# Performance work log

Measured on AMD Instinct MI355X. Metric: run time of the kernel, lower is better.

Reference implementation:

```python
import jax, jax.numpy as jnp
import numpy as np

B, T, E, G, A, D, H1, H2 = 64, 500, 256, 256, 128, 400, 256, 128
MAX_STEPS, R = 500, 5


def setup_inputs() -> dict:
    key = jax.random.key(0)
    ks = jax.random.split(key, 12)
    s = lambda k, shape: jax.random.normal(k, shape, jnp.float32) * 0.05
    return dict(
        enc_feat=jax.random.normal(ks[0], (B, T, E), jnp.float32),
        W_p1=s(ks[1], (D, H1)), b_p1=jnp.zeros((H1,), jnp.float32),
        W_p2=s(ks[2], (H1, H2)), b_p2=jnp.zeros((H2,), jnp.float32),
        # GRU cell (input = prenet_out + context = H2+E)
        W_ix=s(ks[3], (H2 + E, 3 * G)), W_ih=s(ks[4], (G, 3 * G)),
        b_ix=jnp.zeros((3 * G,), jnp.float32), b_ih=jnp.zeros((3 * G,), jnp.float32),
        # Bahdanau MLP attention: v^T tanh(W_dec h + W_enc e + b)
        W_dec=s(ks[5], (G, A)), W_enc=s(ks[6], (E, A)),
        b_attn=jnp.zeros((A,), jnp.float32), v_attn=s(ks[7], (A,)),
        # output projection [G+E] -> D, softmaxed per R chunks
        W_out=s(ks[8], (G + E, D)), b_out=jnp.zeros((D,), jnp.float32),
    )


def reference(enc_feat, W_p1, b_p1, W_p2, b_p2, W_ix, W_ih, b_ix, b_ih,
              W_dec, W_enc, b_attn, v_attn, W_out, b_out):
    # precompute encoder-side attention projection once [B,T,A]
    enc_proj = enc_feat @ W_enc

    def gru_cell(x, h):
        gi = x @ W_ix + b_ix  # [B,3G]
        gh = h @ W_ih + b_ih
        i_r, i_z, i_n = jnp.split(gi, 3, axis=-1)
        h_r, h_z, h_n = jnp.split(gh, 3, axis=-1)
        r = jax.nn.sigmoid(i_r + h_r)
        z = jax.nn.sigmoid(i_z + h_z)
        n = jnp.tanh(i_n + r * h_n)
        return (1.0 - z) * n + z * h

    def step(carry, _):
        pred, h, context = carry
        # prenet (eval: no dropout)
        x = jax.nn.relu(jax.nn.relu(pred @ W_p1 + b_p1) @ W_p2 + b_p2)  # [B,H2]
        h = gru_cell(jnp.concatenate([x, context], axis=-1), h)  # [B,G]
        score = jnp.einsum('bta,a->bt',
                           jnp.tanh(enc_proj + (h @ W_dec + b_attn)[:, None, :]),
                           v_attn)  # [B,T]
        attn = jax.nn.softmax(score, axis=-1)
        context = jnp.einsum('bt,bte->be', attn, enc_feat)  # [B,E]
        raw = jnp.concatenate([h, context], axis=-1) @ W_out + b_out  # [B,D]
        pred = jax.nn.softmax(raw.reshape(B, R, D // R), axis=-1).reshape(B, D)
        return (pred, h, context), (pred, attn)

    init = (jnp.zeros((B, D), enc_feat.dtype),
            jnp.zeros((B, G), enc_feat.dtype),
            jnp.zeros((B, E), enc_feat.dtype))
    _, (pred_seq, attn_record) = jax.lax.scan(step, init, None, length=MAX_STEPS)
    # scan stacks on leading axis: [S,B,.] -> [B,S,.]
    return jnp.transpose(pred_seq, (1, 0, 2)), jnp.transpose(attn_record, (1, 0, 2))
```

## Files before the change

kernel.cpp:

```cpp
#include <hip/hip_runtime.h>
#include <math.h>

constexpr int Bb = 64, Tt = 500, Ee = 256, Aa = 128, Dd = 400;
constexpr int STEPS = 500, Rr = 5;

constexpr size_t WS_ENCPROJ_F = 0;
constexpr size_t WS_STAGE_F   = (size_t)Bb * Tt * Aa;
constexpr size_t WS_CNT_F     = WS_STAGE_F + (size_t)Bb * 2048;
constexpr int SG_L1 = 0, SG_H = 256, SG_SC = 512, SG_CTX = 1024, SG_RAW = 1280;
constexpr int SG_STRIDE = 2048;

__global__ __launch_bounds__(512)
void k_encproj(const float* __restrict__ enc_feat,
               const float* __restrict__ W_enc,
               float* __restrict__ enc_proj) {
  __shared__ float sFeat[16][256];
  const int b = blockIdx.x, tg = blockIdx.y;
  const int t0 = tg * 16;
  const int tid = threadIdx.x;

  #pragma unroll
  for (int i = 0; i < 8; ++i) {
    int idx = tid + i * 512;
    int r = idx >> 8, c = idx & 255;
    int t = t0 + r;
    sFeat[r][c] = (t < Tt) ? enc_feat[((size_t)b * Tt + t) * Ee + c] : 0.0f;
  }
  __syncthreads();

  const int a = tid & 127, tl = tid >> 7;
  float acc0 = 0.f, acc1 = 0.f, acc2 = 0.f, acc3 = 0.f;
  #pragma unroll 4
  for (int k = 0; k < Ee; ++k) {
    float w = W_enc[k * Aa + a];
    acc0 = fmaf(sFeat[tl][k],      w, acc0);
    acc1 = fmaf(sFeat[tl + 4][k],  w, acc1);
    acc2 = fmaf(sFeat[tl + 8][k],  w, acc2);
    acc3 = fmaf(sFeat[tl + 12][k], w, acc3);
  }
  float accs[4] = {acc0, acc1, acc2, acc3};
  #pragma unroll
  for (int i = 0; i < 4; ++i) {
    int t = t0 + tl + 4 * i;
    if (t < Tt) enc_proj[((size_t)b * Tt + t) * Aa + a] = accs[i];
  }
}

__device__ __forceinline__ float sigmoid_acc(float x) {
  float e = __expf(-x);
  return 1.0f / (1.0f + e);
}
__device__ __forceinline__ float tanh_acc(float x) {
  float cx = fminf(9.5f, fmaxf(-9.5f, x));
  float e = __expf(2.0f * cx);
  return (e - 1.0f) / (e + 1.0f);
}
__device__ __forceinline__ float tanh_fast(float x) {
  float cx = fminf(9.5f, fmaxf(-9.5f, x));
  float e = __expf(2.0f * cx);
  return (e - 1.0f) * __builtin_amdgcn_rcpf(e + 1.0f);
}

__device__ __forceinline__ void rowsync(unsigned* __restrict__ cnt, int tid, int& target) {
  __syncthreads();
  target += 4;
  if (tid == 0) {
    __hip_atomic_fetch_add(cnt, 1u, __ATOMIC_RELEASE, __HIP_MEMORY_SCOPE_AGENT);
    while (__hip_atomic_load(cnt, __ATOMIC_RELAXED, __HIP_MEMORY_SCOPE_AGENT) < (unsigned)target) { }
    __threadfence();
  }
  __syncthreads();
}

__global__ __launch_bounds__(512)
void k_decoder(const float* __restrict__ enc_feat,
               const float* __restrict__ enc_proj,
               float* __restrict__ stage, unsigned* __restrict__ cntbase,
               const float* __restrict__ W_p1, const float* __restrict__ b_p1,
               const float* __restrict__ W_p2, const float* __restrict__ b_p2,
               const float* __restrict__ W_ix, const float* __restrict__ W_ih,
               const float* __restrict__ b_ix, const float* __restrict__ b_ih,
               const float* __restrict__ W_dec, const float* __restrict__ b_attn,
               const float* __restrict__ v_attn,
               const float* __restrict__ W_out, const float* __restrict__ b_out,
               float* __restrict__ pred_out, float* __restrict__ attn_out) {
  __shared__ __align__(16) float sPred[400];
  __shared__ __align__(16) float sIn[384];
  __shared__ __align__(16) float sL1[256];
  __shared__ __align__(16) float sCat[512];
  __shared__ __align__(16) float sSd[128];
  __shared__ __align__(16) float sScore[512];
  __shared__ __align__(16) float sRaw[400];
  __shared__ __align__(16) float sTmp[2048];
  __shared__ float sRed[8];

  float* sH = sCat;

  const int bid = blockIdx.x;
  const int r = bid & 63, j = bid >> 6;
  const int tid = threadIdx.x;
  const int lane = tid & 63, wid = tid >> 6;
  const int l4 = tid & 3;

  float* stg = stage + (size_t)r * SG_STRIDE;
  unsigned* cnt = cntbase + r * 64;
  int target = 0;

  for (int i = tid; i < 400; i += 512) sPred[i] = 0.f;
  if (tid < 256) { sH[tid] = 0.f; sIn[128 + tid] = 0.f; }

  float4 vq[8];
  #pragma unroll
  for (int i = 0; i < 8; ++i) vq[i] = *(const float4*)(v_attn + 4 * (l4 + 4 * i));

  float bP1 = 0.f, bR = 0.f, bZ = 0.f, bIN = 0.f, bHN = 0.f;
  if (tid < 64) {
    int c = 64 * j + tid;
    bP1 = b_p1[c];
    bR  = b_ix[c]       + b_ih[c];
    bZ  = b_ix[256 + c] + b_ih[256 + c];
    bIN = b_ix[512 + c];
    bHN = b_ih[512 + c];
  }
  float bP2 = 0.f, bAt = 0.f;
  if (tid < 128) { bP2 = b_p2[tid]; bAt = b_attn[tid]; }
  float bOut = 0.f;
  if (tid < 100) bOut = b_out[100 * j + tid];

  const int p1q = tid & 15, p1s = tid >> 4;
  const int p1k0 = 12 * p1s + min(p1s, 16);
  const int p1k1 = p1k0 + ((p1s < 16) ? 13 : 12);
  const float* p1W = W_p1 + (64 * j + 4 * p1q) + (size_t)p1k0 * 256;
  const int p2q = tid & 31, p2s = tid >> 5;
  const float* p2W = W_p2 + 4 * p2q + (size_t)(16 * p2s) * 128;
  const float* p6W = W_dec + 4 * p2q + (size_t)(16 * p2s) * 128;
  const float* gW = W_ix;
  const float* gx = sIn;
  if (tid < 288) {
    int q = tid % 48, s = tid / 48;
    int g = q >> 4, lq = q & 15;
    gW = W_ix + (size_t)(s * 64) * 768 + (g * 256 + 64 * j + 4 * lq);
    gx = sIn + s * 64;
  } else if (tid < 480) {
    int t2 = tid - 288, q = t2 % 48, s = t2 / 48;
    int g = q >> 4, lq = q & 15;
    gW = W_ih + (size_t)(s * 64) * 768 + (g * 256 + 64 * j + 4 * lq);
    gx = sH + s * 64;
  }
  const bool gAct = tid < 480;
  const int p10q = tid % 25, p10s = tid / 25;
  const int p10k0 = 25 * p10s + min(p10s, 12);
  const int p10k1 = p10k0 + ((p10s < 12) ? 26 : 25);
  const float* p10W = W_out + (100 * j + 4 * p10q) + (size_t)p10k0 * 400;
  const int e9q = tid & 15, t9s = tid >> 4;
  const int t9a = t9s * 16;
  const int t9b = (t9a + 16 < Tt) ? t9a + 16 : Tt;
  const float* fb9 = enc_feat + (size_t)r * Tt * Ee + (64 * j + 4 * e9q);
  const int tt7 = tid >> 2;
  const float* ep7 = enc_proj + ((size_t)r * Tt + (125 * j + tt7)) * Aa;

  __syncthreads();

  for (int t = 0; t < STEPS; ++t) {
    {
      float4 acc = {0.f, 0.f, 0.f, 0.f};
      const float* W = p1W;
      #pragma unroll 8
      for (int k = p1k0; k < p1k1; ++k, W += 256) {
        float xv = sPred[k];
        float4 w = *(const float4*)W;
        acc.x = fmaf(xv, w.x, acc.x); acc.y = fmaf(xv, w.y, acc.y);
        acc.z = fmaf(xv, w.z, acc.z); acc.w = fmaf(xv, w.w, acc.w);
      }
      *(float4*)&sTmp[tid * 4] = acc;
    }
    __syncthreads();
    if (tid < 64) {
      float v = bP1;
      #pragma unroll
      for (int s = 0; s < 32; ++s) v += sTmp[(16 * s + (tid >> 2)) * 4 + (tid & 3)];
      stg[SG_L1 + 64 * j + tid] = fmaxf(v, 0.f);
    }
    rowsync(cnt, tid, target);
    if (tid < 256) sL1[tid] = stg[SG_L1 + tid];
    __syncthreads();

    {
      float4 acc = {0.f, 0.f, 0.f, 0.f};
      const float* W = p2W;
      const float* xp = sL1 + 16 * p2s;
      #pragma unroll 8
      for (int k = 0; k < 16; ++k, W += 128) {
        float xv = xp[k];
        float4 w = *(const float4*)W;
        acc.x = fmaf(xv, w.x, acc.x); acc.y = fmaf(xv, w.y, acc.y);
        acc.z = fmaf(xv, w.z, acc.z); acc.w = fmaf(xv, w.w, acc.w);
      }
      *(float4*)&sTmp[tid * 4] = acc;
    }
    __syncthreads();
    if (tid < 128) {
      float v = bP2;
      #pragma unroll
      for (int s = 0; s < 16; ++s) v += sTmp[(32 * s + (tid >> 2)) * 4 + (tid & 3)];
      sIn[tid] = fmaxf(v, 0.f);
    }
    __syncthreads();

    if (gAct) {
      float4 acc = {0.f, 0.f, 0.f, 0.f};
      const float* W = gW;
      const float* xp = gx;
      #pragma unroll 8
      for (int k = 0; k < 64; ++k, W += 768) {
        float xv = xp[k];
        float4 w = *(const float4*)W;
        acc.x = fmaf(xv, w.x, acc.x); acc.y = fmaf(xv, w.y, acc.y);
        acc.z = fmaf(xv, w.z, acc.z); acc.w = fmaf(xv, w.w, acc.w);
      }
      *(float4*)&sTmp[tid * 4] = acc;
    }
    __syncthreads();
    if (tid < 64) {
      const int cq = tid >> 2, ce = tid & 3;
      float cr = bR, cz = bZ, vin = bIN, vhn = bHN;
      #pragma unroll
      for (int s = 0; s < 6; ++s) {
        cr  += sTmp[(48 * s +      cq) * 4 + ce];
        cz  += sTmp[(48 * s + 16 + cq) * 4 + ce];
        vin += sTmp[(48 * s + 32 + cq) * 4 + ce];
      }
      #pragma unroll
      for (int s = 0; s < 4; ++s) {
        cr  += sTmp[(288 + 48 * s +      cq) * 4 + ce];
        cz  += sTmp[(288 + 48 * s + 16 + cq) * 4 + ce];
        vhn += sTmp[(288 + 48 * s + 32 + cq) * 4 + ce];
      }
      float rg = sigmoid_acc(cr);
      float zg = sigmoid_acc(cz);
      float n  = tanh_acc(vin + rg * vhn);
      stg[SG_H + 64 * j + tid] = (1.f - zg) * n + zg * sH[64 * j + tid];
    }
    rowsync(cnt, tid, target);
    if (tid < 256) sH[tid] = stg[SG_H + tid];
    __syncthreads();

    {
      float4 acc = {0.f, 0.f, 0.f, 0.f};
      const float* W = p6W;
      const float* xp = sH + 16 * p2s;
      #pragma unroll 8
      for (int k = 0; k < 16; ++k, W += 128) {
        float xv = xp[k];
        float4 w = *(const float4*)W;
        acc.x = fmaf(xv, w.x, acc.x); acc.y = fmaf(xv, w.y, acc.y);
        acc.z = fmaf(xv, w.z, acc.z); acc.w = fmaf(xv, w.w, acc.w);
      }
      *(float4*)&sTmp[tid * 4] = acc;
    }
    __syncthreads();
    if (tid < 128) {
      float v = bAt;
      #pragma unroll
      for (int s = 0; s < 16; ++s) v += sTmp[(32 * s + (tid >> 2)) * 4 + (tid & 3)];
      sSd[tid] = v;
    }
    __syncthreads();

    {
      float4 sdq[8];
      #pragma unroll
      for (int i = 0; i < 8; ++i) sdq[i] = *(const float4*)(sSd + 4 * (l4 + 4 * i));
      float acc = 0.f;
      if (tt7 < 125) {
        #pragma unroll
        for (int i = 0; i < 8; ++i) {
          float4 e4 = ((const float4*)ep7)[l4 + 4 * i];
          acc = fmaf(vq[i].x, tanh_fast(e4.x + sdq[i].x), acc);
          acc = fmaf(vq[i].y, tanh_fast(e4.y + sdq[i].y), acc);
          acc = fmaf(vq[i].z, tanh_fast(e4.z + sdq[i].z), acc);
          acc = fmaf(vq[i].w, tanh_fast(e4.w + sdq[i].w), acc);
        }
      }
      acc += __shfl_xor(acc, 1);
      acc += __shfl_xor(acc, 2);
      if (l4 == 0 && tt7 < 125) stg[SG_SC + 125 * j + tt7] = acc;
    }
    rowsync(cnt, tid, target);
    if (tid < Tt) sScore[tid] = stg[SG_SC + tid];
    __syncthreads();

    {
      float val = (tid < Tt) ? sScore[tid] : -3.0e38f;
      float m = val;
      #pragma unroll
      for (int off = 32; off >= 1; off >>= 1) m = fmaxf(m, __shfl_xor(m, off));
      if (lane == 0) sRed[wid] = m;
      __syncthreads();
      float bm = sRed[0];
      #pragma unroll
      for (int w = 1; w < 8; ++w) bm = fmaxf(bm, sRed[w]);
      float e = (tid < Tt) ? __expf(val - bm) : 0.f;
      float ssum = e;
      #pragma unroll
      for (int off = 32; off >= 1; off >>= 1) ssum += __shfl_xor(ssum, off);
      __syncthreads();
      if (lane == 0) sRed[wid] = ssum;
      __syncthreads();
      float S = 0.f;
      #pragma unroll
      for (int w = 0; w < 8; ++w) S += sRed[w];
      if (tid < Tt) {
        float attn = e / S;
        sScore[tid] = attn;
        if (tid >= 125 * j && tid < 125 * (j + 1))
          attn_out[((size_t)r * STEPS + t) * Tt + tid] = attn;
      }
      __syncthreads();
    }

    {
      float4 acc = {0.f, 0.f, 0.f, 0.f};
      #pragma unroll 8
      for (int tt = t9a; tt < t9b; ++tt) {
        float a = sScore[tt];
        float4 f = *(const float4*)(fb9 + (size_t)tt * Ee);
        acc.x = fmaf(a, f.x, acc.x); acc.y = fmaf(a, f.y, acc.y);
        acc.z = fmaf(a, f.z, acc.z); acc.w = fmaf(a, f.w, acc.w);
      }
      *(float4*)&sTmp[tid * 4] = acc;
      __syncthreads();
      if (tid < 64) {
        float v = 0.f;
        #pragma unroll
        for (int s = 0; s < 32; ++s) v += sTmp[(16 * s + (tid >> 2)) * 4 + (tid & 3)];
        stg[SG_CTX + 64 * j + tid] = v;
      }
      rowsync(cnt, tid, target);
      if (tid < 256) {
        float v = stg[SG_CTX + tid];
        sIn[128 + tid] = v;
        sCat[256 + tid] = v;
      }
      __syncthreads();
    }

    if (tid < 500) {
      float4 acc = {0.f, 0.f, 0.f, 0.f};
      const float* W = p10W;
      #pragma unroll 8
      for (int k = p10k0; k < p10k1; ++k, W += 400) {
        float xv = sCat[k];
        float4 w = *(const float4*)W;
        acc.x = fmaf(xv, w.x, acc.x); acc.y = fmaf(xv, w.y, acc.y);
        acc.z = fmaf(xv, w.z, acc.z); acc.w = fmaf(xv, w.w, acc.w);
      }
      *(float4*)&sTmp[tid * 4] = acc;
    }
    __syncthreads();
    if (tid < 100) {
      float v = bOut;
      #pragma unroll
      for (int s = 0; s < 20; ++s) v += sTmp[(25 * s + (tid >> 2)) * 4 + (tid & 3)];
      stg[SG_RAW + 100 * j + tid] = v;
    }
    rowsync(cnt, tid, target);
    if (tid < 400) sRaw[tid] = stg[SG_RAW + tid];
    __syncthreads();

    {
      if (wid < Rr) {
        int d0 = wid * 80 + lane;
        float v0 = sRaw[d0];
        float v1 = (lane < 16) ? sRaw[d0 + 64] : -3.0e38f;
        float m = fmaxf(v0, v1);
        #pragma unroll
        for (int off = 32; off >= 1; off >>= 1) m = fmaxf(m, __shfl_xor(m, off));
        float e0 = __expf(v0 - m);
        float e1 = (lane < 16) ? __expf(v1 - m) : 0.f;
        float s = e0 + e1;
        #pragma unroll
        for (int off = 32; off >= 1; off >>= 1) s += __shfl_xor(s, off);
        float inv = 1.0f / s;
        float p0 = e0 * inv;
        sPred[d0] = p0;
        if (j == 0) pred_out[((size_t)r * STEPS + t) * Dd + d0] = p0;
        if (lane < 16) {
          float p1 = e1 * inv;
          sPred[d0 + 64] = p1;
          if (j == 0) pred_out[((size_t)r * STEPS + t) * Dd + d0 + 64] = p1;
        }
      }
      __syncthreads();
    }
  }
}

extern "C" void kernel_launch(void* const* d_in, const int* in_sizes, int n_in,
                              void* d_out, int out_size, void* d_ws, size_t ws_size,
                              hipStream_t stream) {
  const float* enc_feat = (const float*)d_in[0];
  const float* W_p1  = (const float*)d_in[1];
  const float* b_p1  = (const float*)d_in[2];
  const float* W_p2  = (const float*)d_in[3];
  const float* b_p2  = (const float*)d_in[4];
  const float* W_ix  = (const float*)d_in[5];
  const float* W_ih  = (const float*)d_in[6];
  const float* b_ix  = (const float*)d_in[7];
  const float* b_ih  = (const float*)d_in[8];
  const float* W_dec = (const float*)d_in[9];
  const float* W_enc = (const float*)d_in[10];
  const float* b_attn= (const float*)d_in[11];
  const float* v_attn= (const float*)d_in[12];
  const float* W_out = (const float*)d_in[13];
  const float* b_out = (const float*)d_in[14];

  float* pred_out = (float*)d_out;
  float* attn_out = pred_out + (size_t)Bb * STEPS * Dd;

  float* enc_proj = (float*)d_ws + WS_ENCPROJ_F;
  float* stage    = (float*)d_ws + WS_STAGE_F;
  unsigned* cnt   = (unsigned*)((float*)d_ws + WS_CNT_F);

  hipMemsetAsync(cnt, 0, 64 * 64 * sizeof(unsigned), stream);
  k_encproj<<<dim3(Bb, 32), 512, 0, stream>>>(enc_feat, W_enc, enc_proj);

  void* args[] = {
    (void*)&enc_feat, (void*)&enc_proj, (void*)&stage, (void*)&cnt,
    (void*)&W_p1, (void*)&b_p1, (void*)&W_p2, (void*)&b_p2,
    (void*)&W_ix, (void*)&W_ih, (void*)&b_ix, (void*)&b_ih,
    (void*)&W_dec, (void*)&b_attn, (void*)&v_attn,
    (void*)&W_out, (void*)&b_out, (void*)&pred_out, (void*)&attn_out
  };
  hipLaunchCooperativeKernel(reinterpret_cast<const void*>(k_decoder),
                             dim3(4 * Bb), dim3(512), args, 0, stream);
}
```

Before: 41.89 ms.

## Replicate small matvecs per block and cut cross-block syncs per decoder step

Each of the four blocks per batch row now computes the full prenet layer 1 and output projection redundantly, so the staging exchanges and row barriers for those stages go away. Attention softmax becomes local per block, with only max and sum statistics exchanged, and each block computes a partial context over its own 125 time steps that is then summed across blocks. A double-buffered register prefetch helper replaces the simple weight-streaming dot loops. This trades extra redundant weight traffic and FLOPs per block for fewer grid-level synchronisations per step.

```diff
diff --git a/kernel.cpp b/kernel.cpp
--- a/kernel.cpp
+++ b/kernel.cpp
@@ -7,7 +7,7 @@
 constexpr size_t WS_ENCPROJ_F = 0;
 constexpr size_t WS_STAGE_F   = (size_t)Bb * Tt * Aa;
 constexpr size_t WS_CNT_F     = WS_STAGE_F + (size_t)Bb * 2048;
-constexpr int SG_L1 = 0, SG_H = 256, SG_SC = 512, SG_CTX = 1024, SG_RAW = 1280;
+constexpr int SG_H = 0, SG_STAT = 256, SG_CTXP = 512;
 constexpr int SG_STRIDE = 2048;
 
 __global__ __launch_bounds__(512)
@@ -44,6 +44,55 @@
     int t = t0 + tl + 4 * i;
     if (t < Tt) enc_proj[((size_t)b * Tt + t) * Aa + a] = accs[i];
   }
+}
+
+template<int KS, int NB>
+__device__ __forceinline__ float4 dotq_db(const float* __restrict__ W, const int ldW,
+                                          const float* __restrict__ x) {
+  float4 acc = {0.f, 0.f, 0.f, 0.f};
+  constexpr int NC = KS / NB;
+  constexpr int TL = KS - NC * NB;
+  float4 Abuf[NB], Bbuf[NB > 0 ? NB : 1];
+  if constexpr (NC > 0) {
+    #pragma unroll
+    for (int j = 0; j < NB; ++j) Abuf[j] = *(const float4*)(W + (size_t)j * ldW);
+  }
+  #pragma unroll
+  for (int c = 0; c < NC; ++c) {
+    float4* cur = (c & 1) ? Bbuf : Abuf;
+    float4* nxt = (c & 1) ? Abuf : Bbuf;
+    if (c + 1 < NC) {
+      const float* Wn = W + (size_t)((c + 1) * NB) * ldW;
+      #pragma unroll
+      for (int j = 0; j < NB; ++j) nxt[j] = *(const float4*)(Wn + (size_t)j * ldW);
+    } else if constexpr (TL > 0) {
+      const float* Wn = W + (size_t)(NC * NB) * ldW;
+      #pragma unroll
+      for (int j = 0; j < TL; ++j) nxt[j] = *(const float4*)(Wn + (size_t)j * ldW);
+    }
+    const float* xb = x + c * NB;
+    #pragma unroll
+    for (int j = 0; j < NB; ++j) {
+      float xv = xb[j];
+      acc.x = fmaf(xv, cur[j].x, acc.x); acc.y = fmaf(xv, cur[j].y, acc.y);
+      acc.z = fmaf(xv, cur[j].z, acc.z); acc.w = fmaf(xv, cur[j].w, acc.w);
+    }
+  }
+  if constexpr (TL > 0) {
+    float4* cur = (NC & 1) ? Bbuf : Abuf;
+    if constexpr (NC == 0) {
+      #pragma unroll
+      for (int j = 0; j < TL; ++j) cur[j] = *(const float4*)(W + (size_t)j * ldW);
+    }
+    const float* xb = x + NC * NB;
+    #pragma unroll
+    for (int j = 0; j < TL; ++j) {
+      float xv = xb[j];
+      acc.x = fmaf(xv, cur[j].x, acc.x); acc.y = fmaf(xv, cur[j].y, acc.y);
+      acc.z = fmaf(xv, cur[j].z, acc.z); acc.w = fmaf(xv, cur[j].w, acc.w);
+    }
+  }
+  return acc;
 }
 
 __device__ __forceinline__ float sigmoid_acc(float x) {
@@ -89,7 +138,7 @@
   __shared__ __align__(16) float sL1[256];
   __shared__ __align__(16) float sCat[512];
   __shared__ __align__(16) float sSd[128];
-  __shared__ __align__(16) float sScore[512];
+  __shared__ __align__(16) float sScore[128];
   __shared__ __align__(16) float sRaw[400];
   __shared__ __align__(16) float sTmp[2048];
   __shared__ float sRed[8];
@@ -113,10 +162,11 @@
   #pragma unroll
   for (int i = 0; i < 8; ++i) vq[i] = *(const float4*)(v_attn + 4 * (l4 + 4 * i));
 
-  float bP1 = 0.f, bR = 0.f, bZ = 0.f, bIN = 0.f, bHN = 0.f;
+  float bP1 = 0.f;
+  if (tid < 256) bP1 = b_p1[tid];
+  float bR = 0.f, bZ = 0.f, bIN = 0.f, bHN = 0.f;
   if (tid < 64) {
     int c = 64 * j + tid;
-    bP1 = b_p1[c];
     bR  = b_ix[c]       + b_ih[c];
     bZ  = b_ix[256 + c] + b_ih[256 + c];
     bIN = b_ix[512 + c];
@@ -125,79 +175,46 @@
   float bP2 = 0.f, bAt = 0.f;
   if (tid < 128) { bP2 = b_p2[tid]; bAt = b_attn[tid]; }
   float bOut = 0.f;
-  if (tid < 100) bOut = b_out[100 * j + tid];
-
-  const int p1q = tid & 15, p1s = tid >> 4;
-  const int p1k0 = 12 * p1s + min(p1s, 16);
-  const int p1k1 = p1k0 + ((p1s < 16) ? 13 : 12);
-  const float* p1W = W_p1 + (64 * j + 4 * p1q) + (size_t)p1k0 * 256;
-  const int p2q = tid & 31, p2s = tid >> 5;
-  const float* p2W = W_p2 + 4 * p2q + (size_t)(16 * p2s) * 128;
-  const float* p6W = W_dec + 4 * p2q + (size_t)(16 * p2s) * 128;
+  if (tid < 400) bOut = b_out[tid];
+
+  const float* p1W = W_p1 + 4 * (tid & 63) + (size_t)((tid >> 6) * 50) * 256;
+  const float* p1x = sPred + (tid >> 6) * 50;
+  const float* p2W = W_p2 + 4 * (tid & 31) + (size_t)((tid >> 5) * 16) * 128;
+  const float* p2x = sL1 + (tid >> 5) * 16;
+  const float* p6W = W_dec + 4 * (tid & 31) + (size_t)((tid >> 5) * 16) * 128;
+  const float* p6x = sH + (tid >> 5) * 16;
   const float* gW = W_ix;
   const float* gx = sIn;
-  if (tid < 288) {
+  const bool gAct = tid < 480;
+  if (gAct) {
     int q = tid % 48, s = tid / 48;
-    int g = q >> 4, lq = q & 15;
-    gW = W_ix + (size_t)(s * 64) * 768 + (g * 256 + 64 * j + 4 * lq);
-    gx = sIn + s * 64;
-  } else if (tid < 480) {
-    int t2 = tid - 288, q = t2 % 48, s = t2 / 48;
-    int g = q >> 4, lq = q & 15;
-    gW = W_ih + (size_t)(s * 64) * 768 + (g * 256 + 64 * j + 4 * lq);
-    gx = sH + s * 64;
-  }
-  const bool gAct = tid < 480;
-  const int p10q = tid % 25, p10s = tid / 25;
-  const int p10k0 = 25 * p10s + min(p10s, 12);
-  const int p10k1 = p10k0 + ((p10s < 12) ? 26 : 25);
-  const float* p10W = W_out + (100 * j + 4 * p10q) + (size_t)p10k0 * 400;
-  const int e9q = tid & 15, t9s = tid >> 4;
-  const int t9a = t9s * 16;
-  const int t9b = (t9a + 16 < Tt) ? t9a + 16 : Tt;
-  const float* fb9 = enc_feat + (size_t)r * Tt * Ee + (64 * j + 4 * e9q);
+    int col = 256 * (q >> 4) + 64 * j + 4 * (q & 15);
+    if (s < 6) { gW = W_ix + (size_t)(64 * s) * 768 + col; gx = sIn + 64 * s; }
+    else       { gW = W_ih + (size_t)(64 * (s - 6)) * 768 + col; gx = sH + 64 * (s - 6); }
+  }
+  const int q10 = tid % 100, s10 = tid / 100;
+  const float* p10W = W_out + 4 * q10 + (size_t)(128 * s10) * 400;
+  const float* p10x = sCat + 128 * s10;
   const int tt7 = tid >> 2;
   const float* ep7 = enc_proj + ((size_t)r * Tt + (125 * j + tt7)) * Aa;
+  const int e9q = tid & 63, t9s = tid >> 6;
+  const int t9a = t9s * 16;
+  const float* fb9 = enc_feat + ((size_t)r * Tt + 125 * j + t9a) * Ee + 4 * e9q;
 
   __syncthreads();
 
   for (int t = 0; t < STEPS; ++t) {
-    {
-      float4 acc = {0.f, 0.f, 0.f, 0.f};
-      const float* W = p1W;
-      #pragma unroll 8
-      for (int k = p1k0; k < p1k1; ++k, W += 256) {
-        float xv = sPred[k];
-        float4 w = *(const float4*)W;
-        acc.x = fmaf(xv, w.x, acc.x); acc.y = fmaf(xv, w.y, acc.y);
-        acc.z = fmaf(xv, w.z, acc.z); acc.w = fmaf(xv, w.w, acc.w);
-      }
-      *(float4*)&sTmp[tid * 4] = acc;
-    }
-    __syncthreads();
-    if (tid < 64) {
+    { float4 a = dotq_db<50, 8>(p1W, 256, p1x); *(float4*)&sTmp[tid * 4] = a; }
+    __syncthreads();
+    if (tid < 256) {
       float v = bP1;
       #pragma unroll
-      for (int s = 0; s < 32; ++s) v += sTmp[(16 * s + (tid >> 2)) * 4 + (tid & 3)];
-      stg[SG_L1 + 64 * j + tid] = fmaxf(v, 0.f);
-    }
-    rowsync(cnt, tid, target);
-    if (tid < 256) sL1[tid] = stg[SG_L1 + tid];
-    __syncthreads();
-
-    {
-      float4 acc = {0.f, 0.f, 0.f, 0.f};
-      const float* W = p2W;
-      const float* xp = sL1 + 16 * p2s;
-      #pragma unroll 8
-      for (int k = 0; k < 16; ++k, W += 128) {
-        float xv = xp[k];
-        float4 w = *(const float4*)W;
-        acc.x = fmaf(xv, w.x, acc.x); acc.y = fmaf(xv, w.y, acc.y);
-        acc.z = fmaf(xv, w.z, acc.z); acc.w = fmaf(xv, w.w, acc.w);
-      }
-      *(float4*)&sTmp[tid * 4] = acc;
-    }
+      for (int s = 0; s < 8; ++s) v += sTmp[(64 * s + (tid >> 2)) * 4 + (tid & 3)];
+      sL1[tid] = fmaxf(v, 0.f);
+    }
+    __syncthreads();
+
+    { float4 a = dotq_db<16, 16>(p2W, 128, p2x); *(float4*)&sTmp[tid * 4] = a; }
     __syncthreads();
     if (tid < 128) {
       float v = bP2;
@@ -207,35 +224,20 @@
     }
     __syncthreads();
 
-    if (gAct) {
-      float4 acc = {0.f, 0.f, 0.f, 0.f};
-      const float* W = gW;
-      const float* xp = gx;
-      #pragma unroll 8
-      for (int k = 0; k < 64; ++k, W += 768) {
-        float xv = xp[k];
-        float4 w = *(const float4*)W;
-        acc.x = fmaf(xv, w.x, acc.x); acc.y = fmaf(xv, w.y, acc.y);
-        acc.z = fmaf(xv, w.z, acc.z); acc.w = fmaf(xv, w.w, acc.w);
-      }
-      *(float4*)&sTmp[tid * 4] = acc;
-    }
+    if (gAct) { float4 a = dotq_db<64, 8>(gW, 768, gx); *(float4*)&sTmp[tid * 4] = a; }
     __syncthreads();
     if (tid < 64) {
       const int cq = tid >> 2, ce = tid & 3;
       float cr = bR, cz = bZ, vin = bIN, vhn = bHN;
       #pragma unroll
-      for (int s = 0; s < 6; ++s) {
-        cr  += sTmp[(48 * s +      cq) * 4 + ce];
-        cz  += sTmp[(48 * s + 16 + cq) * 4 + ce];
-        vin += sTmp[(48 * s + 32 + cq) * 4 + ce];
-      }
-      #pragma unroll
-      for (int s = 0; s < 4; ++s) {
-        cr  += sTmp[(288 + 48 * s +      cq) * 4 + ce];
-        cz  += sTmp[(288 + 48 * s + 16 + cq) * 4 + ce];
-        vhn += sTmp[(288 + 48 * s + 32 + cq) * 4 + ce];
-      }
+      for (int s = 0; s < 10; ++s) {
+        cr += sTmp[(48 * s +      cq) * 4 + ce];
+        cz += sTmp[(48 * s + 16 + cq) * 4 + ce];
+      }
+      #pragma unroll
+      for (int s = 0; s < 6; ++s) vin += sTmp[(48 * s + 32 + cq) * 4 + ce];
+      #pragma unroll
+      for (int s = 6; s < 10; ++s) vhn += sTmp[(48 * s + 32 + cq) * 4 + ce];
       float rg = sigmoid_acc(cr);
       float zg = sigmoid_acc(cz);
       float n  = tanh_acc(vin + rg * vhn);
@@ -245,19 +247,7 @@
     if (tid < 256) sH[tid] = stg[SG_H + tid];
     __syncthreads();
 
-    {
-      float4 acc = {0.f, 0.f, 0.f, 0.f};
-      const float* W = p6W;
-      const float* xp = sH + 16 * p2s;
-      #pragma unroll 8
-      for (int k = 0; k < 16; ++k, W += 128) {
-        float xv = xp[k];
-        float4 w = *(const float4*)W;
-        acc.x = fmaf(xv, w.x, acc.x); acc.y = fmaf(xv, w.y, acc.y);
-        acc.z = fmaf(xv, w.z, acc.z); acc.w = fmaf(xv, w.w, acc.w);
-      }
-      *(float4*)&sTmp[tid * 4] = acc;
-    }
+    { float4 a = dotq_db<16, 16>(p6W, 128, p6x); *(float4*)&sTmp[tid * 4] = a; }
     __syncthreads();
     if (tid < 128) {
       float v = bAt;
@@ -284,88 +274,80 @@
       }
       acc += __shfl_xor(acc, 1);
       acc += __shfl_xor(acc, 2);
-      if (l4 == 0 && tt7 < 125) stg[SG_SC + 125 * j + tt7] = acc;
-    }
-    rowsync(cnt, tid, target);
-    if (tid < Tt) sScore[tid] = stg[SG_SC + tid];
-    __syncthreads();
+      if (l4 == 0 && tt7 < 125) sScore[tt7] = acc;
+      __syncthreads();
+    }
 
     {
-      float val = (tid < Tt) ? sScore[tid] : -3.0e38f;
-      float m = val;
-      #pragma unroll
-      for (int off = 32; off >= 1; off >>= 1) m = fmaxf(m, __shfl_xor(m, off));
-      if (lane == 0) sRed[wid] = m;
+      float val = (tid < 125) ? sScore[tid] : -3.0e38f;
+      float lm = val;
+      #pragma unroll
+      for (int off = 32; off >= 1; off >>= 1) lm = fmaxf(lm, __shfl_xor(lm, off));
+      if (lane == 0) sRed[wid] = lm;
       __syncthreads();
       float bm = sRed[0];
       #pragma unroll
       for (int w = 1; w < 8; ++w) bm = fmaxf(bm, sRed[w]);
-      float e = (tid < Tt) ? __expf(val - bm) : 0.f;
-      float ssum = e;
-      #pragma unroll
-      for (int off = 32; off >= 1; off >>= 1) ssum += __shfl_xor(ssum, off);
-      __syncthreads();
-      if (lane == 0) sRed[wid] = ssum;
-      __syncthreads();
-      float S = 0.f;
-      #pragma unroll
-      for (int w = 0; w < 8; ++w) S += sRed[w];
-      if (tid < Tt) {
-        float attn = e / S;
+      float e = (tid < 125) ? __expf(val - bm) : 0.f;
+      float lS = e;
+      #pragma unroll
+      for (int off = 32; off >= 1; off >>= 1) lS += __shfl_xor(lS, off);
+      __syncthreads();
+      if (lane == 0) sRed[wid] = lS;
+      __syncthreads();
+      if (tid == 0) {
+        float S = 0.f;
+        #pragma unroll
+        for (int w = 0; w < 8; ++w) S += sRed[w];
+        stg[SG_STAT + 2 * j] = bm;
+        stg[SG_STAT + 2 * j + 1] = S;
+      }
+      rowsync(cnt, tid, target);
+      float m0 = stg[SG_STAT + 0], S0 = stg[SG_STAT + 1];
+      float m1 = stg[SG_STAT + 2], S1 = stg[SG_STAT + 3];
+      float m2 = stg[SG_STAT + 4], S2 = stg[SG_STAT + 5];
+      float m3 = stg[SG_STAT + 6], S3 = stg[SG_STAT + 7];
+      float M = fmaxf(fmaxf(m0, m1), fmaxf(m2, m3));
+      float Sg = S0 * __expf(m0 - M) + S1 * __expf(m1 - M) +
+                 S2 * __expf(m2 - M) + S3 * __expf(m3 - M);
+      if (tid < 125) {
+        float attn = __expf(sScore[tid] - M) / Sg;
         sScore[tid] = attn;
-        if (tid >= 125 * j && tid < 125 * (j + 1))
-          attn_out[((size_t)r * STEPS + t) * Tt + tid] = attn;
+        attn_out[((size_t)r * STEPS + t) * Tt + 125 * j + tid] = attn;
       }
       __syncthreads();
     }
 
     {
-      float4 acc = {0.f, 0.f, 0.f, 0.f};
-      #pragma unroll 8
-      for (int tt = t9a; tt < t9b; ++tt) {
-        float a = sScore[tt];
-        float4 f = *(const float4*)(fb9 + (size_t)tt * Ee);
-        acc.x = fmaf(a, f.x, acc.x); acc.y = fmaf(a, f.y, acc.y);
-        acc.z = fmaf(a, f.z, acc.z); acc.w = fmaf(a, f.w, acc.w);
-      }
-      *(float4*)&sTmp[tid * 4] = acc;
-      __syncthreads();
-      if (tid < 64) {
+      float4 part;
+      if (t9s < 7) part = dotq_db<16, 16>(fb9, Ee, sScore + t9a);
+      else         part = dotq_db<13, 13>(fb9, Ee, sScore + t9a);
+      *(float4*)&sTmp[tid * 4] = part;
+      __syncthreads();
+      if (tid < 256) {
         float v = 0.f;
         #pragma unroll
-        for (int s = 0; s < 32; ++s) v += sTmp[(16 * s + (tid >> 2)) * 4 + (tid & 3)];
-        stg[SG_CTX + 64 * j + tid] = v;
+        for (int s = 0; s < 8; ++s) v += sTmp[(64 * s + (tid >> 2)) * 4 + (tid & 3)];
+        stg[SG_CTXP + 256 * j + tid] = v;
       }
       rowsync(cnt, tid, target);
       if (tid < 256) {
-        float v = stg[SG_CTX + tid];
+        float v = stg[SG_CTXP + tid] + stg[SG_CTXP + 256 + tid] +
+                  stg[SG_CTXP + 512 + tid] + stg[SG_CTXP + 768 + tid];
         sIn[128 + tid] = v;
         sCat[256 + tid] = v;
       }
       __syncthreads();
     }
 
-    if (tid < 500) {
-      float4 acc = {0.f, 0.f, 0.f, 0.f};
-      const float* W = p10W;
-      #pragma unroll 8
-      for (int k = p10k0; k < p10k1; ++k, W += 400) {
-        float xv = sCat[k];
-        float4 w = *(const float4*)W;
-        acc.x = fmaf(xv, w.x, acc.x); acc.y = fmaf(xv, w.y, acc.y);
-        acc.z = fmaf(xv, w.z, acc.z); acc.w = fmaf(xv, w.w, acc.w);
-      }
-      *(float4*)&sTmp[tid * 4] = acc;
-    }
-    __syncthreads();
-    if (tid < 100) {
+    if (tid < 400) { float4 a = dotq_db<128, 8>(p10W, 400, p10x); *(float4*)&sTmp[tid * 4] = a; }
+    __syncthreads();
+    if (tid < 400) {
       float v = bOut;
       #pragma unroll
-      for (int s = 0; s < 20; ++s) v += sTmp[(25 * s + (tid >> 2)) * 4 + (tid & 3)];
-      stg[SG_RAW + 100 * j + tid] = v;
-    }
-    rowsync(cnt, tid, target);
-    if (tid < 400) sRaw[tid] = stg[SG_RAW + tid];
+      for (int s = 0; s < 4; ++s) v += sTmp[(100 * s + (tid >> 2)) * 4 + (tid & 3)];
+      sRaw[tid] = v;
+    }
     __syncthreads();
 
     {
@@ -422,7 +404,7 @@
   float* stage    = (float*)d_ws + WS_STAGE_F;
   unsigned* cnt   = (unsigned*)((float*)d_ws + WS_CNT_F);
 
-  hipMemsetAsync(cnt, 0, 64 * 64 * sizeof(unsigned), stream);
+  (void)hipMemsetAsync(cnt, 0, 64 * 64 * sizeof(unsigned), stream);
   k_encproj<<<dim3(Bb, 32), 512, 0, stream>>>(enc_feat, W_enc, enc_proj);
 
   void* args[] = {
@@ -432,6 +414,6 @@
     (void*)&W_dec, (void*)&b_attn, (void*)&v_attn,
     (void*)&W_out, (void*)&b_out, (void*)&pred_out, (void*)&attn_out
   };
-  hipLaunchCooperativeKernel(reinterpret_cast<const void*>(k_decoder),
-                             dim3(4 * Bb), dim3(512), args, 0, stream);
-}
+  (void)hipLaunchCooperativeKernel(reinterpret_cast<const void*>(k_decoder),
+                                   dim3(4 * Bb), dim3(512), args, 0, stream);
+}
```

Result: slower. 95.94 ms (+129.0%).
